# Performance work log

Hardware: AMD Instinct MI355X
Metric: run time of the kernel (lower is better)

Reference implementation:

```python
import jax, jax.numpy as jnp
import numpy as np

N, IN, OUT, R, E = 20000, 768, 768, 8, 320000


def setup_inputs() -> dict:
    key = jax.random.key(0)
    ks = jax.random.split(key, 9)
    x = jax.random.normal(ks[0], (N, IN), dtype=jnp.float32)
    edge_index = jax.random.randint(ks[1], (2, E), 0, N, dtype=jnp.int64)
    edge_type = jax.random.randint(ks[2], (E,), 0, R, dtype=jnp.int64)
    s1 = 1.0 / np.sqrt(IN)
    s2 = 1.0 / np.sqrt(OUT)
    W1 = jax.random.normal(ks[3], (R, IN, OUT), dtype=jnp.float32) * s1
    root1 = jax.random.normal(ks[4], (IN, OUT), dtype=jnp.float32) * s1
    b1 = jnp.zeros((OUT,), dtype=jnp.float32)
    W2 = jax.random.normal(ks[5], (R, OUT, OUT), dtype=jnp.float32) * s2
    root2 = jax.random.normal(ks[6], (OUT, OUT), dtype=jnp.float32) * s2
    b2 = jnp.zeros((OUT,), dtype=jnp.float32)
    return {"x": x, "edge_index": edge_index, "edge_type": edge_type,
            "W1": W1, "root1": root1, "b1": b1,
            "W2": W2, "root2": root2, "b2": b2}


def _rgcn_conv(x, src, dst, etype, W, root, b):
    # PyG RGCNConv: per-relation mean aggregation of neighbor features,
    # then relation-specific linear transform, plus root weight and bias.
    # mean(x_j @ W_r) == mean(x_j) @ W_r, so aggregate first, transform after.
    num_nodes = x.shape[0]
    num_rel = W.shape[0]
    x_src = x[src]                                  # [E, d_in]
    seg = dst * num_rel + etype                     # composite (node, relation) id
    sums = jax.ops.segment_sum(x_src, seg, num_segments=num_nodes * num_rel)
    cnt = jax.ops.segment_sum(jnp.ones((src.shape[0],), dtype=x.dtype), seg,
                              num_segments=num_nodes * num_rel)
    mean = sums / jnp.maximum(cnt, 1.0)[:, None]    # [N*R, d_in]
    mean = mean.reshape(num_nodes, num_rel, -1)     # [N, R, d_in]
    out = jnp.einsum('nri,rio->no', mean, W)        # relation-batched matmul
    return out + x @ root + b


def reference(x, edge_index, edge_type, W1, root1, b1, W2, root2, b2):
    src, dst = edge_index[0], edge_index[1]
    h = _rgcn_conv(x, src, dst, edge_type, W1, root1, b1)
    h = jax.nn.relu(h)
    out = _rgcn_conv(h, src, dst, edge_type, W2, root2, b2)
    return out
```

## Files before the change

kernel.cpp:

```cpp
#include <hip/hip_runtime.h>
#include <hip/hip_bf16.h>
#include <stdint.h>

#define N_NODES 20000
#define DIM     768
#define NREL    8
#define NEDGE   320000
#define NSEG    (N_NODES * NREL)
#define GKA     6144
#define GK      6912
#define NT_TILES (GK / 64)
#define NPW     2

typedef short short8 __attribute__((ext_vector_type(8)));
typedef float f32x4  __attribute__((ext_vector_type(4)));

__device__ __forceinline__ void async_load16(const void* g, void* l) {
  __builtin_amdgcn_global_load_lds((const __attribute__((address_space(1))) void*)g,
                                   (__attribute__((address_space(3))) void*)l,
                                   16, 0, 0);
}

__device__ __forceinline__ int imin(int a, int b) { return a < b ? a : b; }

__device__ __forceinline__ float bf_lo(uint32_t v) {
  return __builtin_bit_cast(float, v << 16);
}
__device__ __forceinline__ float bf_hi(uint32_t v) {
  return __builtin_bit_cast(float, v & 0xffff0000u);
}
__device__ __forceinline__ uint32_t pack_bf16x2(float a, float b) {
  uint32_t lo = __builtin_bit_cast(unsigned short, __float2bfloat16(a));
  uint32_t hi = __builtin_bit_cast(unsigned short, __float2bfloat16(b));
  return lo | (hi << 16);
}

__global__ void seg_count_kernel(const int* __restrict__ dst, const int* __restrict__ et,
                                 int* __restrict__ segcnt, int e_cnt) {
  int e = blockIdx.x * 256 + threadIdx.x;
  if (e < e_cnt) atomicAdd(&segcnt[dst[e] * NREL + et[e]], 1);
}

__global__ void block_scan_kernel(const int* __restrict__ in, int* __restrict__ out,
                                  int* __restrict__ partials, int n) {
  __shared__ int wsum[16];
  const int t = threadIdx.x, lane = t & 63, wave = t >> 6;
  const int i = blockIdx.x * 1024 + t;
  int v = (i < n) ? in[i] : 0;
  int s = v;
#pragma unroll
  for (int off = 1; off < 64; off <<= 1) {
    int u = __shfl_up(s, off, 64);
    if (lane >= off) s += u;
  }
  if (lane == 63) wsum[wave] = s;
  __syncthreads();
  if (t < 16) {
    int w = wsum[t];
#pragma unroll
    for (int off = 1; off < 16; off <<= 1) {
      int u = __shfl_up(w, off, 64);
      if (t >= off) w += u;
    }
    wsum[t] = w;
  }
  __syncthreads();
  const int basew = (wave > 0) ? wsum[wave - 1] : 0;
  if (i < n) out[i] = basew + s - v;
  if (t == 1023) partials[blockIdx.x] = wsum[15];
}

__global__ void partial_scan_kernel(int* __restrict__ partials, int nb) {
  const int lane = threadIdx.x & 63;
  int carry = 0;
  for (int base = 0; base < nb; base += 64) {
    const int i = base + lane;
    int v = (i < nb) ? partials[i] : 0;
    int s = v;
#pragma unroll
    for (int off = 1; off < 64; off <<= 1) {
      int u = __shfl_up(s, off, 64);
      if (lane >= off) s += u;
    }
    if (i < nb) partials[i] = carry + s - v;
    carry += __shfl(s, 63, 64);
  }
}

__global__ void add_offsets_kernel(int* __restrict__ soffs, const int* __restrict__ partials,
                                   int* __restrict__ cursor, int n) {
  const int i = blockIdx.x * 1024 + threadIdx.x;
  if (i < n) {
    const int v = soffs[i] + partials[blockIdx.x];
    soffs[i] = v;
    cursor[i] = v;
  }
  if (i == 0) soffs[n] = NEDGE;
}

__global__ void seg_scatter_kernel(const int* __restrict__ src, const int* __restrict__ dst,
                                   const int* __restrict__ et, int* __restrict__ cursor,
                                   int* __restrict__ es, int e_cnt) {
  int e = blockIdx.x * 256 + threadIdx.x;
  if (e < e_cnt) {
    const int seg = dst[e] * NREL + et[e];
    const int p = atomicAdd(&cursor[seg], 1);
    es[p] = src[e];
  }
}

__global__ void cvt_bf16_kernel(const float4* __restrict__ in, ushort4* __restrict__ out, int n4) {
  int i = blockIdx.x * 256 + threadIdx.x;
  if (i < n4) {
    float4 f = in[i];
    ushort4 r;
    r.x = __builtin_bit_cast(unsigned short, __float2bfloat16(f.x));
    r.y = __builtin_bit_cast(unsigned short, __float2bfloat16(f.y));
    r.z = __builtin_bit_cast(unsigned short, __float2bfloat16(f.z));
    r.w = __builtin_bit_cast(unsigned short, __float2bfloat16(f.w));
    out[i] = r;
  }
}

__global__ void transpose_w_kernel(const float* __restrict__ src, __hip_bfloat16* __restrict__ dst,
                                   int rows, int col_off) {
  __shared__ float tile[32][33];
  const int c0 = blockIdx.x * 32;
  const int r0 = blockIdx.y * 32;
  const int tx = threadIdx.x, ty = threadIdx.y;
  for (int i = ty; i < 32; i += 8) {
    int r = r0 + i, c = c0 + tx;
    tile[i][tx] = (r < rows) ? src[(size_t)r * DIM + c] : 0.f;
  }
  __syncthreads();
  for (int i = ty; i < 32; i += 8) {
    int c = c0 + i, r = r0 + tx;
    if (r < rows)
      dst[(size_t)c * GK + col_off + r] = __float2bfloat16(tile[tx][i]);
  }
}

__global__ __launch_bounds__(256) void aggregate_kernel(
    const __hip_bfloat16* __restrict__ feat,
    const int* __restrict__ soffs, const int* __restrict__ es,
    __hip_bfloat16* __restrict__ Abuf,
    int node_base, int rows) {
  const int t = threadIdx.x;
  const int lane = t & 63;
  const int wave = t >> 6;
  const int boff = lane * 8;

  int nloc = (blockIdx.x * 4 + wave) * NPW;
  for (int it = 0; it < NPW; ++it, ++nloc) {
    if (nloc >= rows) return;
    const int n = node_base + nloc;
    char* Ab = (char*)(Abuf + (size_t)nloc * GKA);
#pragma unroll
    for (int r = 0; r < NREL; ++r) {
      const int beg = soffs[n * NREL + r], end = soffs[n * NREL + r + 1];
      float acc[12];
#pragma unroll
      for (int i = 0; i < 12; ++i) acc[i] = 0.f;
      int e = beg;
      for (; e + 2 <= end; e += 2) {
        const int s0 = es[e], s1 = es[e + 1];
        const char* p0 = (const char*)(feat + (size_t)s0 * DIM) + boff;
        const char* p1 = (const char*)(feat + (size_t)s1 * DIM) + boff;
        const uint2 a0 = *(const uint2*)(p0);
        const uint2 a1 = *(const uint2*)(p0 + 512);
        const uint2 a2 = *(const uint2*)(p0 + 1024);
        const uint2 b0 = *(const uint2*)(p1);
        const uint2 b1 = *(const uint2*)(p1 + 512);
        const uint2 b2 = *(const uint2*)(p1 + 1024);
        acc[0]  += bf_lo(a0.x); acc[1]  += bf_hi(a0.x);
        acc[2]  += bf_lo(a0.y); acc[3]  += bf_hi(a0.y);
        acc[4]  += bf_lo(a1.x); acc[5]  += bf_hi(a1.x);
        acc[6]  += bf_lo(a1.y); acc[7]  += bf_hi(a1.y);
        acc[8]  += bf_lo(a2.x); acc[9]  += bf_hi(a2.x);
        acc[10] += bf_lo(a2.y); acc[11] += bf_hi(a2.y);
        acc[0]  += bf_lo(b0.x); acc[1]  += bf_hi(b0.x);
        acc[2]  += bf_lo(b0.y); acc[3]  += bf_hi(b0.y);
        acc[4]  += bf_lo(b1.x); acc[5]  += bf_hi(b1.x);
        acc[6]  += bf_lo(b1.y); acc[7]  += bf_hi(b1.y);
        acc[8]  += bf_lo(b2.x); acc[9]  += bf_hi(b2.x);
        acc[10] += bf_lo(b2.y); acc[11] += bf_hi(b2.y);
      }
      if (e < end) {
        const int s0 = es[e];
        const char* p0 = (const char*)(feat + (size_t)s0 * DIM) + boff;
        const uint2 a0 = *(const uint2*)(p0);
        const uint2 a1 = *(const uint2*)(p0 + 512);
        const uint2 a2 = *(const uint2*)(p0 + 1024);
        acc[0]  += bf_lo(a0.x); acc[1]  += bf_hi(a0.x);
        acc[2]  += bf_lo(a0.y); acc[3]  += bf_hi(a0.y);
        acc[4]  += bf_lo(a1.x); acc[5]  += bf_hi(a1.x);
        acc[6]  += bf_lo(a1.y); acc[7]  += bf_hi(a1.y);
        acc[8]  += bf_lo(a2.x); acc[9]  += bf_hi(a2.x);
        acc[10] += bf_lo(a2.y); acc[11] += bf_hi(a2.y);
      }
      const float inv = 1.f / fmaxf((float)(end - beg), 1.f);
      uint2 o0, o1, o2;
      o0.x = pack_bf16x2(acc[0] * inv, acc[1] * inv);
      o0.y = pack_bf16x2(acc[2] * inv, acc[3] * inv);
      o1.x = pack_bf16x2(acc[4] * inv, acc[5] * inv);
      o1.y = pack_bf16x2(acc[6] * inv, acc[7] * inv);
      o2.x = pack_bf16x2(acc[8] * inv, acc[9] * inv);
      o2.y = pack_bf16x2(acc[10] * inv, acc[11] * inv);
      char* dst = Ab + r * (DIM * 2);
      *(uint2*)(dst + boff) = o0;
      *(uint2*)(dst + boff + 512) = o1;
      *(uint2*)(dst + boff + 1024) = o2;
    }
  }
}

__global__ __launch_bounds__(512, 2) void gemm_kernel(
    const __hip_bfloat16* __restrict__ A,
    const __hip_bfloat16* __restrict__ feat,
    const __hip_bfloat16* __restrict__ BT,
    const float* __restrict__ bias,
    __hip_bfloat16* __restrict__ outb,
    float* __restrict__ outf,
    int mvalid, int node_base, int mode) {
  __shared__ __hip_bfloat16 lds[2][2][2][128][64];

  const int t = threadIdx.x;
  const int lane = t & 63;
  const int wid = t >> 6;
  const int wave_m = wid >> 2;
  const int wave_n = wid & 3;
  const int ml = lane & 15;
  const int quad = lane >> 4;
  const int sw8 = ml & 7;
  const int lsub = lane >> 3;
  const int lg = (lane & 7) ^ lsub;
  const int wrow = wid * 8;

  const int nbx = gridDim.x;
  const int nwg = nbx * gridDim.y;
  const int lid = blockIdx.y * nbx + blockIdx.x;
  const int q = nwg >> 3, r = nwg & 7;
  const int xcd = lid & 7, off = lid >> 3;
  const int swz = (xcd < r ? xcd * (q + 1) : r * (q + 1) + (xcd - r) * q) + off;
  const int m0 = (swz / nbx) * 256;
  const int n0 = (swz % nbx) * 256;

  const char* cA = (const char*)A;
  const char* cF = (const char*)feat;
  const char* cB = (const char*)BT;
  uint32_t offA[2][2], offF[2][2], offB[2][2];
#pragma unroll
  for (int h = 0; h < 2; ++h)
#pragma unroll
    for (int i = 0; i < 2; ++i) {
      const int srow = h * 128 + i * 64 + wrow + lsub;
      const int ar = imin(m0 + srow, mvalid - 1);
      const int fr = imin(node_base + m0 + srow, N_NODES - 1);
      offA[h][i] = (uint32_t)ar * (uint32_t)(GKA * 2) + (uint32_t)(lg * 16);
      offF[h][i] = (uint32_t)fr * (uint32_t)(DIM * 2) + (uint32_t)(lg * 16);
      offB[h][i] = (uint32_t)(n0 + srow) * (uint32_t)(GK * 2) + (uint32_t)(lg * 16);
    }

#define VMCNT(N) asm volatile("s_waitcnt vmcnt(" #N ")" ::: "memory")
#define LGKM0()  asm volatile("s_waitcnt lgkmcnt(0)" ::: "memory")
#define BAR()    asm volatile("s_barrier" ::: "memory")

#define STAGE_A(BUF, H, TS) do {                                                   \
    const char* _s0 = ((TS) < 96) ? cA + offA[H][0] + (size_t)(TS) * 128           \
                                  : cF + offF[H][0] + (size_t)((TS) - 96) * 128;   \
    const char* _s1 = ((TS) < 96) ? cA + offA[H][1] + (size_t)(TS) * 128           \
                                  : cF + offF[H][1] + (size_t)((TS) - 96) * 128;   \
    async_load16(_s0, &lds[BUF][0][H][wrow][0]);                                   \
    async_load16(_s1, &lds[BUF][0][H][64 + wrow][0]);                              \
  } while (0)

#define STAGE_B(BUF, H, TS) do {                                                   \
    async_load16(cB + offB[H][0] + (size_t)(TS) * 128, &lds[BUF][1][H][wrow][0]);  \
    async_load16(cB + offB[H][1] + (size_t)(TS) * 128, &lds[BUF][1][H][64 + wrow][0]); \
  } while (0)

#define LOAD_A(BUF, MH)                                                            \
  _Pragma("unroll") for (int mi = 0; mi < 4; ++mi)                                 \
  _Pragma("unroll") for (int kk = 0; kk < 2; ++kk)                                 \
    a[mi][kk] = *(const short8*)&lds[BUF][0][MH][wave_m * 64 + mi * 16 + ml]       \
                                              [((kk * 4 + quad) ^ sw8) * 8];

#define LOAD_B(BUF, NH, DST)                                                       \
  _Pragma("unroll") for (int ni = 0; ni < 2; ++ni)                                 \
  _Pragma("unroll") for (int kk = 0; kk < 2; ++kk)                                 \
    DST[ni][kk] = *(const short8*)&lds[BUF][1][NH][wave_n * 32 + ni * 16 + ml]     \
                                                 [((kk * 4 + quad) ^ sw8) * 8];

#define DO_MFMA(MH, NH, BREG)                                                      \
  _Pragma("unroll") for (int mi = 0; mi < 4; ++mi)                                 \
  _Pragma("unroll") for (int ni = 0; ni < 2; ++ni) {                               \
    acc[MH][NH][mi][ni] = __builtin_amdgcn_mfma_f32_16x16x32_bf16(                 \
        a[mi][0], BREG[ni][0], acc[MH][NH][mi][ni], 0, 0, 0);                      \
    acc[MH][NH][mi][ni] = __builtin_amdgcn_mfma_f32_16x16x32_bf16(                 \
        a[mi][1], BREG[ni][1], acc[MH][NH][mi][ni], 0, 0, 0);                      \
  }

  f32x4 acc[2][2][4][2] = {};
  short8 a[4][2];
  short8 b0[2][2], b1[2][2];

  STAGE_A(0, 0, 0);
  STAGE_B(0, 0, 0);
  STAGE_A(0, 1, 0);
  STAGE_B(0, 1, 0);
  STAGE_A(1, 0, 1);
  STAGE_B(1, 0, 1);
  VMCNT(4);
  BAR();

#pragma unroll 2
  for (int T = 0; T < NT_TILES; ++T) {
    const int buf = T & 1;
    const int ts1 = (T + 1 < NT_TILES) ? T + 1 : NT_TILES - 1;
    const int ts2 = (T + 2 < NT_TILES) ? T + 2 : NT_TILES - 1;
    VMCNT(4);
    LOAD_A(buf, 0);
    LOAD_B(buf, 0, b0);
    STAGE_A(buf ^ 1, 1, ts1);
    STAGE_B(buf ^ 1, 1, ts1);
    BAR(); LGKM0();
    __builtin_amdgcn_s_setprio(1);
    DO_MFMA(0, 0, b0);
    __builtin_amdgcn_s_setprio(0);
    BAR();
    LOAD_B(buf, 1, b1);
    BAR(); LGKM0();
    __builtin_amdgcn_s_setprio(1);
    DO_MFMA(0, 1, b1);
    __builtin_amdgcn_s_setprio(0);
    BAR();
    LOAD_A(buf, 1);
    STAGE_A(buf, 0, ts2);
    BAR(); LGKM0();
    __builtin_amdgcn_s_setprio(1);
    DO_MFMA(1, 0, b0);
    __builtin_amdgcn_s_setprio(0);
    BAR();
    VMCNT(6);
    STAGE_B(buf, 0, ts2);
    BAR(); LGKM0();
    __builtin_amdgcn_s_setprio(1);
    DO_MFMA(1, 1, b1);
    __builtin_amdgcn_s_setprio(0);
    BAR();
  }
  VMCNT(0);

#undef VMCNT
#undef LGKM0
#undef BAR
#undef STAGE_A
#undef STAGE_B
#undef LOAD_A
#undef LOAD_B
#undef DO_MFMA

  float bcol[2][2];
#pragma unroll
  for (int nh = 0; nh < 2; ++nh)
#pragma unroll
    for (int ni = 0; ni < 2; ++ni)
      bcol[nh][ni] = bias[n0 + nh * 128 + wave_n * 32 + ni * 16 + ml];

#pragma unroll
  for (int mh = 0; mh < 2; ++mh)
#pragma unroll
    for (int mi = 0; mi < 4; ++mi)
#pragma unroll
      for (int rr = 0; rr < 4; ++rr) {
        const int row = m0 + mh * 128 + wave_m * 64 + mi * 16 + quad * 4 + rr;
        if (row < mvalid) {
          const size_t orow = (size_t)(node_base + row) * DIM;
#pragma unroll
          for (int nh = 0; nh < 2; ++nh)
#pragma unroll
            for (int ni = 0; ni < 2; ++ni) {
              const int col = n0 + nh * 128 + wave_n * 32 + ni * 16 + ml;
              const float v = acc[mh][nh][mi][ni][rr] + bcol[nh][ni];
              if (mode == 0) outb[orow + col] = __float2bfloat16(fmaxf(v, 0.f));
              else           outf[orow + col] = v;
            }
        }
      }
}

extern "C" void kernel_launch(void* const* d_in, const int* in_sizes, int n_in,
                              void* d_out, int out_size, void* d_ws, size_t ws_size,
                              hipStream_t stream) {
  const float* x     = (const float*)d_in[0];
  const int*   eidx  = (const int*)d_in[1];
  const int*   etype = (const int*)d_in[2];
  const float* W1    = (const float*)d_in[3];
  const float* root1 = (const float*)d_in[4];
  const float* b1    = (const float*)d_in[5];
  const float* W2    = (const float*)d_in[6];
  const float* root2 = (const float*)d_in[7];
  const float* b2    = (const float*)d_in[8];
  float* out = (float*)d_out;
  const int* esrc_in = eidx;
  const int* edst_in = eidx + NEDGE;

  char* p = (char*)d_ws;
  auto alloc = [&](size_t bytes) -> char* {
    char* r = p;
    p += (bytes + 255) & ~(size_t)255;
    return r;
  };
  __hip_bfloat16* xb  = (__hip_bfloat16*)alloc((size_t)N_NODES * DIM * 2);
  __hip_bfloat16* hb  = (__hip_bfloat16*)alloc((size_t)N_NODES * DIM * 2);
  __hip_bfloat16* w1t = (__hip_bfloat16*)alloc((size_t)DIM * GK * 2);
  __hip_bfloat16* w2t = (__hip_bfloat16*)alloc((size_t)DIM * GK * 2);
  int* segcnt   = (int*)alloc((size_t)NSEG * 4);
  int* soffs    = (int*)alloc((size_t)(NSEG + 1) * 4);
  int* cursor   = (int*)alloc((size_t)NSEG * 4);
  int* partials = (int*)alloc(256 * 4);
  int* es       = (int*)alloc((size_t)NEDGE * 4);
  size_t used = (size_t)(p - (char*)d_ws);
  size_t remain = (ws_size > used) ? (ws_size - used) : 0;
  long long caprows_ll = (long long)(remain / ((size_t)GKA * 2));
  int caprows = (int)((caprows_ll / 128) * 128);
  if (caprows > 20096) caprows = 20096;
  if (caprows < 128) caprows = 128;
  __hip_bfloat16* Abuf = (__hip_bfloat16*)p;

  const int NB = (NSEG + 1023) / 1024;
  hipMemsetAsync(segcnt, 0, (size_t)NSEG * 4, stream);
  seg_count_kernel<<<(NEDGE + 255) / 256, 256, 0, stream>>>(edst_in, etype, segcnt, NEDGE);
  block_scan_kernel<<<NB, 1024, 0, stream>>>(segcnt, soffs, partials, NSEG);
  partial_scan_kernel<<<1, 64, 0, stream>>>(partials, NB);
  add_offsets_kernel<<<NB, 1024, 0, stream>>>(soffs, partials, cursor, NSEG);
  seg_scatter_kernel<<<(NEDGE + 255) / 256, 256, 0, stream>>>(esrc_in, edst_in, etype, cursor, es, NEDGE);

  cvt_bf16_kernel<<<((N_NODES * DIM / 4) + 255) / 256, 256, 0, stream>>>(
      (const float4*)x, (ushort4*)xb, N_NODES * DIM / 4);
  dim3 tb(32, 8);
  transpose_w_kernel<<<dim3(DIM / 32, (NREL * DIM) / 32), tb, 0, stream>>>(W1, w1t, NREL * DIM, 0);
  transpose_w_kernel<<<dim3(DIM / 32, DIM / 32), tb, 0, stream>>>(root1, w1t, DIM, NREL * DIM);
  transpose_w_kernel<<<dim3(DIM / 32, (NREL * DIM) / 32), tb, 0, stream>>>(W2, w2t, NREL * DIM, 0);
  transpose_w_kernel<<<dim3(DIM / 32, DIM / 32), tb, 0, stream>>>(root2, w2t, DIM, NREL * DIM);

  for (int base = 0; base < N_NODES; base += caprows) {
    int rows = N_NODES - base; if (rows > caprows) rows = caprows;
    int agrid = (rows + 4 * NPW - 1) / (4 * NPW);
    aggregate_kernel<<<agrid, 256, 0, stream>>>(xb, soffs, es, Abuf, base, rows);
    dim3 grid(DIM / 256, (rows + 255) / 256);
    gemm_kernel<<<grid, 512, 0, stream>>>(Abuf, xb, w1t, b1, hb, nullptr, rows, base, 0);
  }
  for (int base = 0; base < N_NODES; base += caprows) {
    int rows = N_NODES - base; if (rows > caprows) rows = caprows;
    int agrid = (rows + 4 * NPW - 1) / (4 * NPW);
    aggregate_kernel<<<agrid, 256, 0, stream>>>(hb, soffs, es, Abuf, base, rows);
    dim3 grid(DIM / 256, (rows + 255) / 256);
    gemm_kernel<<<grid, 512, 0, stream>>>(Abuf, hb, w2t, b2, nullptr, out, rows, base, 1);
  }
}
```

Measured before the change: 1.142 ms.

## Copy root features into A buffer and restructure GEMM LDS pipeline with double-buffered A fragments

The aggregate kernel now appends each node's own feature row to its A-buffer row, so the GEMM reads a single contiguous K=6912 operand instead of switching between the aggregated buffer and the feature array. The GEMM main loop is rescheduled so that A and B fragments for the next sub-tile are loaded from LDS while the current MFMAs run. Two A register sets are kept, explicit lgkmcnt waits are dropped, and vmcnt thresholds are retuned. This removes the per-stage branch and the LDS-read stalls in exchange for more register pressure and an extra 1.5KB write per node in aggregation.

```diff
diff --git a/kernel.cpp b/kernel.cpp
--- a/kernel.cpp
+++ b/kernel.cpp
@@ -154,7 +154,7 @@
   for (int it = 0; it < NPW; ++it, ++nloc) {
     if (nloc >= rows) return;
     const int n = node_base + nloc;
-    char* Ab = (char*)(Abuf + (size_t)nloc * GKA);
+    char* Ab = (char*)(Abuf + (size_t)nloc * GK);
 #pragma unroll
     for (int r = 0; r < NREL; ++r) {
       const int beg = soffs[n * NREL + r], end = soffs[n * NREL + r + 1];
@@ -211,12 +211,16 @@
       *(uint2*)(dst + boff + 512) = o1;
       *(uint2*)(dst + boff + 1024) = o2;
     }
+    const char* fsrc = (const char*)(feat + (size_t)n * DIM);
+    char* fdst = Ab + GKA * 2;
+    *(uint2*)(fdst + boff) = *(const uint2*)(fsrc + boff);
+    *(uint2*)(fdst + boff + 512) = *(const uint2*)(fsrc + boff + 512);
+    *(uint2*)(fdst + boff + 1024) = *(const uint2*)(fsrc + boff + 1024);
   }
 }
 
 __global__ __launch_bounds__(512, 2) void gemm_kernel(
     const __hip_bfloat16* __restrict__ A,
-    const __hip_bfloat16* __restrict__ feat,
     const __hip_bfloat16* __restrict__ BT,
     const float* __restrict__ bias,
     __hip_bfloat16* __restrict__ outb,
@@ -246,44 +250,38 @@
   const int n0 = (swz % nbx) * 256;
 
   const char* cA = (const char*)A;
-  const char* cF = (const char*)feat;
   const char* cB = (const char*)BT;
-  uint32_t offA[2][2], offF[2][2], offB[2][2];
+  uint32_t offA[2][2], offB[2][2];
 #pragma unroll
   for (int h = 0; h < 2; ++h)
 #pragma unroll
     for (int i = 0; i < 2; ++i) {
       const int srow = h * 128 + i * 64 + wrow + lsub;
       const int ar = imin(m0 + srow, mvalid - 1);
-      const int fr = imin(node_base + m0 + srow, N_NODES - 1);
-      offA[h][i] = (uint32_t)ar * (uint32_t)(GKA * 2) + (uint32_t)(lg * 16);
-      offF[h][i] = (uint32_t)fr * (uint32_t)(DIM * 2) + (uint32_t)(lg * 16);
+      offA[h][i] = (uint32_t)ar * (uint32_t)(GK * 2) + (uint32_t)(lg * 16);
       offB[h][i] = (uint32_t)(n0 + srow) * (uint32_t)(GK * 2) + (uint32_t)(lg * 16);
     }
 
 #define VMCNT(N) asm volatile("s_waitcnt vmcnt(" #N ")" ::: "memory")
-#define LGKM0()  asm volatile("s_waitcnt lgkmcnt(0)" ::: "memory")
 #define BAR()    asm volatile("s_barrier" ::: "memory")
 
-#define STAGE_A(BUF, H, TS) do {                                                   \
-    const char* _s0 = ((TS) < 96) ? cA + offA[H][0] + (size_t)(TS) * 128           \
-                                  : cF + offF[H][0] + (size_t)((TS) - 96) * 128;   \
-    const char* _s1 = ((TS) < 96) ? cA + offA[H][1] + (size_t)(TS) * 128           \
-                                  : cF + offF[H][1] + (size_t)((TS) - 96) * 128;   \
-    async_load16(_s0, &lds[BUF][0][H][wrow][0]);                                   \
-    async_load16(_s1, &lds[BUF][0][H][64 + wrow][0]);                              \
+#define STG_A(SB, H, TS) do {                                                      \
+    const char* _p = cA + (size_t)(TS) * 128;                                      \
+    async_load16(_p + offA[H][0], &lds[SB][0][H][wrow][0]);                        \
+    async_load16(_p + offA[H][1], &lds[SB][0][H][64 + wrow][0]);                   \
   } while (0)
 
-#define STAGE_B(BUF, H, TS) do {                                                   \
-    async_load16(cB + offB[H][0] + (size_t)(TS) * 128, &lds[BUF][1][H][wrow][0]);  \
-    async_load16(cB + offB[H][1] + (size_t)(TS) * 128, &lds[BUF][1][H][64 + wrow][0]); \
+#define STG_B(SB, H, TS) do {                                                      \
+    const char* _p = cB + (size_t)(TS) * 128;                                      \
+    async_load16(_p + offB[H][0], &lds[SB][1][H][wrow][0]);                        \
+    async_load16(_p + offB[H][1], &lds[SB][1][H][64 + wrow][0]);                   \
   } while (0)
 
-#define LOAD_A(BUF, MH)                                                            \
+#define LOAD_A(BUF, MH, DST)                                                       \
   _Pragma("unroll") for (int mi = 0; mi < 4; ++mi)                                 \
   _Pragma("unroll") for (int kk = 0; kk < 2; ++kk)                                 \
-    a[mi][kk] = *(const short8*)&lds[BUF][0][MH][wave_m * 64 + mi * 16 + ml]       \
-                                              [((kk * 4 + quad) ^ sw8) * 8];
+    DST[mi][kk] = *(const short8*)&lds[BUF][0][MH][wave_m * 64 + mi * 16 + ml]     \
+                                                 [((kk * 4 + quad) ^ sw8) * 8];
 
 #define LOAD_B(BUF, NH, DST)                                                       \
   _Pragma("unroll") for (int ni = 0; ni < 2; ++ni)                                 \
@@ -291,71 +289,73 @@
     DST[ni][kk] = *(const short8*)&lds[BUF][1][NH][wave_n * 32 + ni * 16 + ml]     \
                                                  [((kk * 4 + quad) ^ sw8) * 8];
 
-#define DO_MFMA(MH, NH, BREG)                                                      \
+#define DO_MFMA(MH, NH, AF, BF)                                                    \
   _Pragma("unroll") for (int mi = 0; mi < 4; ++mi)                                 \
   _Pragma("unroll") for (int ni = 0; ni < 2; ++ni) {                               \
     acc[MH][NH][mi][ni] = __builtin_amdgcn_mfma_f32_16x16x32_bf16(                 \
-        a[mi][0], BREG[ni][0], acc[MH][NH][mi][ni], 0, 0, 0);                      \
+        AF[mi][0], BF[ni][0], acc[MH][NH][mi][ni], 0, 0, 0);                       \
     acc[MH][NH][mi][ni] = __builtin_amdgcn_mfma_f32_16x16x32_bf16(                 \
-        a[mi][1], BREG[ni][1], acc[MH][NH][mi][ni], 0, 0, 0);                      \
+        AF[mi][1], BF[ni][1], acc[MH][NH][mi][ni], 0, 0, 0);                       \
   }
 
   f32x4 acc[2][2][4][2] = {};
-  short8 a[4][2];
+  short8 aA[4][2], aB[4][2];
   short8 b0[2][2], b1[2][2];
 
-  STAGE_A(0, 0, 0);
-  STAGE_B(0, 0, 0);
-  STAGE_A(0, 1, 0);
-  STAGE_B(0, 1, 0);
-  STAGE_A(1, 0, 1);
-  STAGE_B(1, 0, 1);
-  VMCNT(4);
+  STG_A(0, 0, 0); STG_B(0, 0, 0);
+  STG_B(0, 1, 0);
+  STG_A(0, 1, 0);
+  STG_A(1, 0, 1); STG_B(1, 0, 1);
+  STG_B(1, 1, 1);
+  STG_A(1, 1, 1);
+  VMCNT(12);
   BAR();
-
-#pragma unroll 2
+  LOAD_A(0, 0, aA);
+  LOAD_B(0, 0, b0);
+  VMCNT(8);
+  BAR();
+
   for (int T = 0; T < NT_TILES; ++T) {
     const int buf = T & 1;
-    const int ts1 = (T + 1 < NT_TILES) ? T + 1 : NT_TILES - 1;
     const int ts2 = (T + 2 < NT_TILES) ? T + 2 : NT_TILES - 1;
+    VMCNT(8);
+    LOAD_B(buf, 1, b1);
+    BAR();
+    __builtin_amdgcn_s_setprio(1);
+    DO_MFMA(0, 0, aA, b0);
+    __builtin_amdgcn_s_setprio(0);
+    BAR();
     VMCNT(4);
-    LOAD_A(buf, 0);
-    LOAD_B(buf, 0, b0);
-    STAGE_A(buf ^ 1, 1, ts1);
-    STAGE_B(buf ^ 1, 1, ts1);
-    BAR(); LGKM0();
+    STG_A(buf, 0, ts2);
+    STG_B(buf, 0, ts2);
+    LOAD_A(buf, 1, aB);
+    BAR();
     __builtin_amdgcn_s_setprio(1);
-    DO_MFMA(0, 0, b0);
+    DO_MFMA(0, 1, aA, b1);
     __builtin_amdgcn_s_setprio(0);
     BAR();
-    LOAD_B(buf, 1, b1);
-    BAR(); LGKM0();
+    STG_B(buf, 1, ts2);
+    LOAD_A(buf ^ 1, 0, aA);
+    BAR();
     __builtin_amdgcn_s_setprio(1);
-    DO_MFMA(0, 1, b1);
+    DO_MFMA(1, 0, aB, b0);
     __builtin_amdgcn_s_setprio(0);
     BAR();
-    LOAD_A(buf, 1);
-    STAGE_A(buf, 0, ts2);
-    BAR(); LGKM0();
+    VMCNT(8);
+    STG_A(buf, 1, ts2);
+    LOAD_B(buf ^ 1, 0, b0);
+    BAR();
     __builtin_amdgcn_s_setprio(1);
-    DO_MFMA(1, 0, b0);
+    DO_MFMA(1, 1, aB, b1);
     __builtin_amdgcn_s_setprio(0);
     BAR();
-    VMCNT(6);
-    STAGE_B(buf, 0, ts2);
-    BAR(); LGKM0();
-    __builtin_amdgcn_s_setprio(1);
-    DO_MFMA(1, 1, b1);
-    __builtin_amdgcn_s_setprio(0);
-    BAR();
   }
   VMCNT(0);
 
 #undef VMCNT
-#undef LGKM0
 #undef BAR
-#undef STAGE_A
-#undef STAGE_B
+#undef STG_A
+#undef STG_B
 #undef LOAD_A
 #undef LOAD_B
 #undef DO_MFMA
@@ -422,7 +422,7 @@
   int* es       = (int*)alloc((size_t)NEDGE * 4);
   size_t used = (size_t)(p - (char*)d_ws);
   size_t remain = (ws_size > used) ? (ws_size - used) : 0;
-  long long caprows_ll = (long long)(remain / ((size_t)GKA * 2));
+  long long caprows_ll = (long long)(remain / ((size_t)GK * 2));
   int caprows = (int)((caprows_ll / 128) * 128);
   if (caprows > 20096) caprows = 20096;
   if (caprows < 128) caprows = 128;
@@ -449,13 +449,13 @@
     int agrid = (rows + 4 * NPW - 1) / (4 * NPW);
     aggregate_kernel<<<agrid, 256, 0, stream>>>(xb, soffs, es, Abuf, base, rows);
     dim3 grid(DIM / 256, (rows + 255) / 256);
-    gemm_kernel<<<grid, 512, 0, stream>>>(Abuf, xb, w1t, b1, hb, nullptr, rows, base, 0);
+    gemm_kernel<<<grid, 512, 0, stream>>>(Abuf, w1t, b1, hb, nullptr, rows, base, 0);
   }
   for (int base = 0; base < N_NODES; base += caprows) {
     int rows = N_NODES - base; if (rows > caprows) rows = caprows;
     int agrid = (rows + 4 * NPW - 1) / (4 * NPW);
     aggregate_kernel<<<agrid, 256, 0, stream>>>(hb, soffs, es, Abuf, base, rows);
     dim3 grid(DIM / 256, (rows + 255) / 256);
-    gemm_kernel<<<grid, 512, 0, stream>>>(Abuf, hb, w2t, b2, nullptr, out, rows, base, 1);
-  }
-}
+    gemm_kernel<<<grid, 512, 0, stream>>>(Abuf, w2t, b2, nullptr, out, rows, base, 1);
+  }
+}
```

Result: no change. 1.124 ms (-1.5%).
